# Optimization experiments

Hardware: AMD Instinct MI355X
Metric: run time of the kernel (lower is better)

The kernel has to match this reference:

```python
import jax, jax.numpy as jnp
import numpy as np

CHANNEL = 64
RATIO = 8
C1 = CHANNEL // RATIO


def setup_inputs() -> dict:
    key = jax.random.key(0)
    ks = jax.random.split(key, 8)
    b, c, h, w = 2, CHANNEL, 96, 96
    X = jax.random.normal(ks[0], (b, c, h, w), dtype=jnp.float32)
    Y = jax.random.normal(ks[1], (b, c, h, w), dtype=jnp.float32)
    # 1x1 conv weights (stored as [out, in]) + biases, Kaiming-ish scale
    s = 1.0 / np.sqrt(c)
    Wq = jax.random.uniform(ks[2], (C1, c), jnp.float32, -s, s)
    bq = jax.random.uniform(ks[3], (C1,), jnp.float32, -s, s)
    Wk = jax.random.uniform(ks[4], (C1, c), jnp.float32, -s, s)
    bk = jax.random.uniform(ks[5], (C1,), jnp.float32, -s, s)
    Wv = jax.random.uniform(ks[6], (c, c), jnp.float32, -s, s)
    bv = jax.random.uniform(ks[7], (c,), jnp.float32, -s, s)
    return {"X": X, "Y": Y, "Wq": Wq, "bq": bq, "Wk": Wk, "bk": bk, "Wv": Wv, "bv": bv}


def reference(X, Y, Wq, bq, Wk, bk, Wv, bv):
    b, c, h, w = Y.shape
    n = h * w
    # 1x1 convs as channel contractions -> [b, n, c_out]
    Xf = X.reshape(b, c, n)                       # [b, c, n]
    q = jnp.einsum('oc,bcn->bno', Wq, Xf) + bq    # [b, n, c1]
    k = jnp.einsum('oc,bcn->bno', Wk, Xf) + bk    # [b, n, c1]
    v = jnp.einsum('oc,bcn->bno', Wv, Y.reshape(b, c, n)) + bv  # [b, n, c]
    scores = jnp.einsum('bic,bjc->bij', q, k)     # [b, n, n]
    # NOTE: softmax over dim=1 (the first n axis), as in the original module
    a = jax.nn.softmax(scores, axis=1)
    x = jnp.einsum('bij,bjc->bic', a, v)          # [b, n, c]
    x = x.transpose(0, 2, 1).reshape(b, c, h, w)
    return Y + x
```

## Files before the change

### kernel.cpp

```cpp
#include <hip/hip_runtime.h>

#define NPOS 9216
#define NB 2
#define CCH 64
#define VZP 40

typedef __attribute__((ext_vector_type(8))) short short8;
typedef __attribute__((ext_vector_type(4))) float f32x4;

#define LOG2E 1.4426950408889634f

__device__ __forceinline__ ushort f2bf(float x) {
    unsigned u = __builtin_bit_cast(unsigned, x);
    u += 0x7FFFu + ((u >> 16) & 1u);
    return (ushort)(u >> 16);
}

__device__ __forceinline__ unsigned cvt_pk_bf16(float lo, float hi) {
    unsigned r;
    asm("v_cvt_pk_bf16_f32 %0, %1, %2" : "=v"(r) : "v"(lo), "v"(hi));
    return r;
}

__global__ __launch_bounds__(256) void qkv_kernel(
    const float* __restrict__ X, const float* __restrict__ Y,
    const float* __restrict__ Wq, const float* __restrict__ bq,
    const float* __restrict__ Wk, const float* __restrict__ bk,
    const float* __restrict__ Wv, const float* __restrict__ bv,
    ushort* __restrict__ qb, ushort* __restrict__ kb, float* __restrict__ v,
    float* __restrict__ out)
{
    __shared__ float wqkT[1024];
    __shared__ float wvT[4096];
    int tid = threadIdx.x;
    for (int idx = tid; idx < 1024; idx += 256) {
        int c = idx >> 4, o = idx & 15;
        wqkT[idx] = (o < 8) ? Wq[o * 64 + c] : Wk[(o - 8) * 64 + c];
    }
    for (int idx = tid; idx < 4096; idx += 256) {
        int c = idx >> 6, o = idx & 63;
        wvT[idx] = Wv[o * 64 + c];
    }
    __syncthreads();

    int p = tid & 63, s = tid >> 6;
    int base = blockIdx.x * 64;
    int b = base / NPOS;
    int n = (base % NPOS) + p;

    float va[16], qk[8];
    #pragma unroll
    for (int o = 0; o < 16; ++o) va[o] = bv[s * 16 + o];
    #pragma unroll
    for (int o = 0; o < 8; ++o) qk[o] = 0.f;
    if (s == 0) {
        #pragma unroll
        for (int o = 0; o < 8; ++o) qk[o] = bq[o];
    } else if (s == 1) {
        #pragma unroll
        for (int o = 0; o < 8; ++o) qk[o] = bk[o];
    }

    const float* Xb = X + (size_t)b * CCH * NPOS + n;
    const float* Yb = Y + (size_t)b * CCH * NPOS + n;
    float* ob = out + (size_t)b * CCH * NPOS + n;
    for (int c = 0; c < 64; ++c) {
        float yv = Yb[(size_t)c * NPOS];
        ob[(size_t)c * NPOS] = yv;
        const float4* wv4 = (const float4*)(wvT + c * 64 + s * 16);
        #pragma unroll
        for (int o4 = 0; o4 < 4; ++o4) {
            float4 wv = wv4[o4];
            va[o4*4+0] += wv.x * yv; va[o4*4+1] += wv.y * yv;
            va[o4*4+2] += wv.z * yv; va[o4*4+3] += wv.w * yv;
        }
        if (s < 2) {
            float xv = Xb[(size_t)c * NPOS];
            const float4* wq4 = (const float4*)(wqkT + c * 16 + s * 8);
            float4 w0 = wq4[0], w1 = wq4[1];
            qk[0] += w0.x * xv; qk[1] += w0.y * xv;
            qk[2] += w0.z * xv; qk[3] += w0.w * xv;
            qk[4] += w1.x * xv; qk[5] += w1.y * xv;
            qk[6] += w1.z * xv; qk[7] += w1.w * xv;
        }
    }
    float4* vdst = (float4*)(v + ((size_t)b * NPOS + n) * 64 + s * 16);
    #pragma unroll
    for (int o4 = 0; o4 < 4; ++o4)
        vdst[o4] = make_float4(va[o4*4], va[o4*4+1], va[o4*4+2], va[o4*4+3]);
    if (s < 2) {
        if (s == 0) {
            #pragma unroll
            for (int o = 0; o < 8; ++o) qk[o] *= LOG2E;
        }
        short8 row;
        #pragma unroll
        for (int o = 0; o < 8; ++o) row[o] = (short)f2bf(qk[o]);
        ushort* dst = (s == 0 ? qb : kb) + ((size_t)b * NPOS + n) * 8;
        *(short8*)dst = row;
    }
}

__global__ __launch_bounds__(256) void zpass_kernel(
    const ushort* __restrict__ qb, const ushort* __restrict__ kb,
    float* __restrict__ Z)
{
    int tid = threadIdx.x;
    int w = tid >> 6, l = tid & 63;
    int il = l & 15, g = l >> 4;
    int b = blockIdx.z;
    int jb = blockIdx.x * 64 + w * 16;
    const short8 zero8 = {0,0,0,0,0,0,0,0};
    const f32x4 cz = {0.f,0.f,0.f,0.f};

    short8 kf = zero8;
    if (g == 0) kf = *(const short8*)(kb + ((size_t)b * NPOS + jb + il) * 8);

    float za[4] = {0.f, 0.f, 0.f, 0.f};
    const ushort* qrow = qb + ((size_t)b * NPOS + blockIdx.y * 2304 + il) * 8;
    for (int is = 0; is < 144; ++is) {
        short8 qf = *(const short8*)(qrow + (size_t)is * 128);
        if (g != 0) qf = zero8;
        f32x4 sv = __builtin_amdgcn_mfma_f32_16x16x32_bf16(kf, qf, cz, 0, 0, 0);
        za[0] += __builtin_amdgcn_exp2f(sv[0]);
        za[1] += __builtin_amdgcn_exp2f(sv[1]);
        za[2] += __builtin_amdgcn_exp2f(sv[2]);
        za[3] += __builtin_amdgcn_exp2f(sv[3]);
    }
    #pragma unroll
    for (int r = 0; r < 4; ++r) {
        float x = za[r];
        x += __shfl_xor(x, 1, 16);
        x += __shfl_xor(x, 2, 16);
        x += __shfl_xor(x, 4, 16);
        x += __shfl_xor(x, 8, 16);
        za[r] = x;
    }
    if (il == 0) {
        #pragma unroll
        for (int r = 0; r < 4; ++r)
            atomicAdd(&Z[(size_t)b * NPOS + jb + g * 4 + r], za[r]);
    }
}

__global__ __launch_bounds__(256) void scalevT_kernel(
    const float* __restrict__ v, const float* __restrict__ Z,
    ushort* __restrict__ VzT)
{
    int tid = threadIdx.x;
    int p = tid & 63, s = tid >> 6;
    int base = blockIdx.x * 64;
    int b = base / NPOS;
    int n = (base % NPOS) + p;
    float rz = 1.0f / Z[(size_t)b * NPOS + n];
    const float4* vr = (const float4*)(v + ((size_t)b * NPOS + n) * 64 + s * 16);
    ushort* dst = VzT + (size_t)b * CCH * NPOS + n;
    #pragma unroll
    for (int q4 = 0; q4 < 4; ++q4) {
        float4 a = vr[q4];
        size_t c0 = s * 16 + q4 * 4;
        dst[(c0 + 0) * NPOS] = f2bf(a.x * rz);
        dst[(c0 + 1) * NPOS] = f2bf(a.y * rz);
        dst[(c0 + 2) * NPOS] = f2bf(a.z * rz);
        dst[(c0 + 3) * NPOS] = f2bf(a.w * rz);
    }
}

__global__ __launch_bounds__(256) void pass2_kernel(
    const ushort* __restrict__ qb, const ushort* __restrict__ kb,
    const ushort* __restrict__ VzT, float* __restrict__ out)
{
    __shared__ ushort vz_lds[2][64 * VZP];
    __shared__ ushort p_lds[4][512];
    int tid = threadIdx.x;
    int w = tid >> 6, l = tid & 63;
    int il = l & 15, g = l >> 4;
    int b = blockIdx.z;
    int ibase = blockIdx.x * 64 + w * 16;
    int j0 = blockIdx.y * 2304;

    const short8 zero8 = {0,0,0,0,0,0,0,0};
    const f32x4 cz = {0.f,0.f,0.f,0.f};

    short8 qf = zero8;
    if (g == 0) qf = *(const short8*)(qb + ((size_t)b * NPOS + ibase + il) * 8);

    f32x4 acc[4];
    #pragma unroll
    for (int cg = 0; cg < 4; ++cg) acc[cg] = cz;

    const ushort* kbb = kb + (size_t)b * NPOS * 8;
    int sc = tid >> 2, sslot = tid & 3;
    const ushort* vsrc = VzT + (size_t)b * CCH * NPOS + (size_t)sc * NPOS + j0 + sslot * 8;

    *(float4*)&vz_lds[0][sc * VZP + sslot * 8] = *(const float4*)vsrc;
    __syncthreads();

    int swz = (il >> 1) & 3;
    ushort* pw = p_lds[w];

    for (int st = 0; st < 72; ++st) {
        int jb = j0 + st * 32;
        int cur = st & 1;
        bool more = (st + 1) < 72;
        float4 nv = {0.f,0.f,0.f,0.f};
        if (more) nv = *(const float4*)(vsrc + (size_t)(st + 1) * 32);

        short8 kf0 = zero8, kf1 = zero8;
        if (g == 0) {
            kf0 = *(const short8*)(kbb + (size_t)(jb + il) * 8);
            kf1 = *(const short8*)(kbb + (size_t)(jb + 16 + il) * 8);
        }
        f32x4 s0 = __builtin_amdgcn_mfma_f32_16x16x32_bf16(kf0, qf, cz, 0, 0, 0);
        f32x4 s1 = __builtin_amdgcn_mfma_f32_16x16x32_bf16(kf1, qf, cz, 0, 0, 0);

        int rowoff = il * 32 + (g & 1) * 4;
        {
            int stored = ((g >> 1) ^ swz);
            unsigned u01 = cvt_pk_bf16(__builtin_amdgcn_exp2f(s0[0]),
                                       __builtin_amdgcn_exp2f(s0[1]));
            unsigned u23 = cvt_pk_bf16(__builtin_amdgcn_exp2f(s0[2]),
                                       __builtin_amdgcn_exp2f(s0[3]));
            *(unsigned*)&pw[rowoff + stored * 8 + 0] = u01;
            *(unsigned*)&pw[rowoff + stored * 8 + 2] = u23;
        }
        {
            int stored = ((2 | (g >> 1)) ^ swz);
            unsigned u01 = cvt_pk_bf16(__builtin_amdgcn_exp2f(s1[0]),
                                       __builtin_amdgcn_exp2f(s1[1]));
            unsigned u23 = cvt_pk_bf16(__builtin_amdgcn_exp2f(s1[2]),
                                       __builtin_amdgcn_exp2f(s1[3]));
            *(unsigned*)&pw[rowoff + stored * 8 + 0] = u01;
            *(unsigned*)&pw[rowoff + stored * 8 + 2] = u23;
        }

        short8 pf = *(short8*)&pw[il * 32 + ((g ^ swz) * 8)];

        #pragma unroll
        for (int cg = 0; cg < 4; ++cg) {
            short8 af = *(short8*)&vz_lds[cur][(cg * 16 + il) * VZP + g * 8];
            acc[cg] = __builtin_amdgcn_mfma_f32_16x16x32_bf16(af, pf, acc[cg], 0, 0, 0);
        }

        if (more) *(float4*)&vz_lds[cur ^ 1][sc * VZP + sslot * 8] = nv;
        __syncthreads();
    }

    float* ob = out + (size_t)b * CCH * NPOS + ibase + il;
    #pragma unroll
    for (int cg = 0; cg < 4; ++cg) {
        #pragma unroll
        for (int r = 0; r < 4; ++r) {
            int c = cg * 16 + g * 4 + r;
            atomicAdd(ob + (size_t)c * NPOS, acc[cg][r]);
        }
    }
}

extern "C" void kernel_launch(void* const* d_in, const int* in_sizes, int n_in,
                              void* d_out, int out_size, void* d_ws, size_t ws_size,
                              hipStream_t stream) {
    const float* X  = (const float*)d_in[0];
    const float* Y  = (const float*)d_in[1];
    const float* Wq = (const float*)d_in[2];
    const float* bq = (const float*)d_in[3];
    const float* Wk = (const float*)d_in[4];
    const float* bk = (const float*)d_in[5];
    const float* Wv = (const float*)d_in[6];
    const float* bv = (const float*)d_in[7];

    char* ws = (char*)d_ws;
    ushort* qb  = (ushort*)(ws);
    ushort* kbw = (ushort*)(ws + 294912);
    ushort* VzT = (ushort*)(ws + 589824);
    float*  v   = (float*) (ws + 2949120);
    float*  Z   = (float*) (ws + 7667712);

    hipMemsetAsync(Z, 0, (size_t)NB * NPOS * sizeof(float), stream);

    qkv_kernel<<<288, 256, 0, stream>>>(X, Y, Wq, bq, Wk, bk, Wv, bv,
                                        qb, kbw, v, (float*)d_out);
    zpass_kernel<<<dim3(144, 4, NB), 256, 0, stream>>>(qb, kbw, Z);
    scalevT_kernel<<<288, 256, 0, stream>>>(v, Z, VzT);
    pass2_kernel<<<dim3(144, 4, NB), 256, 0, stream>>>(qb, kbw, VzT, (float*)d_out);
}
```

Baseline: 207.6 us.

## Fold 1/Z into probabilities, widen pass2 tiles to 32 rows by 64 columns

V is now written directly as transposed bf16 by the QKV kernel, and the scale-by-1/Z step moves into pass2, where each exp score is multiplied by a precomputed reciprocal. This replaces the full scalevT pass and the fp32 V round trip with a tiny reciprocal kernel. pass2 now gives each wave 32 query rows over 64 j steps, using XOR-swizzled LDS tiles, prefetched K fragments and a split of 8 along j instead of 4. The larger tiles cut loop and sync overhead per MFMA, at the cost of more registers, more atomic adds per output and bf16 rounding applied to p/Z instead of V/Z.

New measurement: 218.9 us. 1.05x slower.

```diff
diff --git a/kernel.cpp b/kernel.cpp
--- a/kernel.cpp
+++ b/kernel.cpp
@@ -3,7 +3,9 @@
 #define NPOS 9216
 #define NB 2
 #define CCH 64
-#define VZP 40
+#define JSPLIT 8
+#define JCHUNK (NPOS / JSPLIT)
+#define NSTEP (JCHUNK / 64)
 
 typedef __attribute__((ext_vector_type(8))) short short8;
 typedef __attribute__((ext_vector_type(4))) float f32x4;
@@ -27,11 +29,11 @@
     const float* __restrict__ Wq, const float* __restrict__ bq,
     const float* __restrict__ Wk, const float* __restrict__ bk,
     const float* __restrict__ Wv, const float* __restrict__ bv,
-    ushort* __restrict__ qb, ushort* __restrict__ kb, float* __restrict__ v,
-    float* __restrict__ out)
+    ushort* __restrict__ qb, ushort* __restrict__ kb,
+    ushort* __restrict__ vT, float* __restrict__ out)
 {
     __shared__ float wqkT[1024];
-    __shared__ float wvT[4096];
+    __shared__ float wvTs[4096];
     int tid = threadIdx.x;
     for (int idx = tid; idx < 1024; idx += 256) {
         int c = idx >> 4, o = idx & 15;
@@ -39,7 +41,7 @@
     }
     for (int idx = tid; idx < 4096; idx += 256) {
         int c = idx >> 6, o = idx & 63;
-        wvT[idx] = Wv[o * 64 + c];
+        wvTs[idx] = Wv[o * 64 + c];
     }
     __syncthreads();
 
@@ -67,7 +69,7 @@
     for (int c = 0; c < 64; ++c) {
         float yv = Yb[(size_t)c * NPOS];
         ob[(size_t)c * NPOS] = yv;
-        const float4* wv4 = (const float4*)(wvT + c * 64 + s * 16);
+        const float4* wv4 = (const float4*)(wvTs + c * 64 + s * 16);
         #pragma unroll
         for (int o4 = 0; o4 < 4; ++o4) {
             float4 wv = wv4[o4];
@@ -84,10 +86,10 @@
             qk[6] += w1.z * xv; qk[7] += w1.w * xv;
         }
     }
-    float4* vdst = (float4*)(v + ((size_t)b * NPOS + n) * 64 + s * 16);
-    #pragma unroll
-    for (int o4 = 0; o4 < 4; ++o4)
-        vdst[o4] = make_float4(va[o4*4], va[o4*4+1], va[o4*4+2], va[o4*4+3]);
+    ushort* vdst = vT + (size_t)b * CCH * NPOS + n;
+    #pragma unroll
+    for (int o = 0; o < 16; ++o)
+        vdst[(size_t)(s * 16 + o) * NPOS] = f2bf(va[o]);
     if (s < 2) {
         if (s == 0) {
             #pragma unroll
@@ -118,6 +120,7 @@
 
     float za[4] = {0.f, 0.f, 0.f, 0.f};
     const ushort* qrow = qb + ((size_t)b * NPOS + blockIdx.y * 2304 + il) * 8;
+    #pragma unroll 4
     for (int is = 0; is < 144; ++is) {
         short8 qf = *(const short8*)(qrow + (size_t)is * 128);
         if (g != 0) qf = zero8;
@@ -143,118 +146,144 @@
     }
 }
 
-__global__ __launch_bounds__(256) void scalevT_kernel(
-    const float* __restrict__ v, const float* __restrict__ Z,
-    ushort* __restrict__ VzT)
+__global__ __launch_bounds__(256) void recipz_kernel(
+    const float* __restrict__ Z, float* __restrict__ rz)
 {
-    int tid = threadIdx.x;
-    int p = tid & 63, s = tid >> 6;
-    int base = blockIdx.x * 64;
-    int b = base / NPOS;
-    int n = (base % NPOS) + p;
-    float rz = 1.0f / Z[(size_t)b * NPOS + n];
-    const float4* vr = (const float4*)(v + ((size_t)b * NPOS + n) * 64 + s * 16);
-    ushort* dst = VzT + (size_t)b * CCH * NPOS + n;
-    #pragma unroll
-    for (int q4 = 0; q4 < 4; ++q4) {
-        float4 a = vr[q4];
-        size_t c0 = s * 16 + q4 * 4;
-        dst[(c0 + 0) * NPOS] = f2bf(a.x * rz);
-        dst[(c0 + 1) * NPOS] = f2bf(a.y * rz);
-        dst[(c0 + 2) * NPOS] = f2bf(a.z * rz);
-        dst[(c0 + 3) * NPOS] = f2bf(a.w * rz);
-    }
+    int i = blockIdx.x * 256 + threadIdx.x;
+    rz[i] = __builtin_amdgcn_rcpf(Z[i]);
 }
 
 __global__ __launch_bounds__(256) void pass2_kernel(
     const ushort* __restrict__ qb, const ushort* __restrict__ kb,
-    const ushort* __restrict__ VzT, float* __restrict__ out)
+    const ushort* __restrict__ vT, const float* __restrict__ rz,
+    float* __restrict__ out)
 {
-    __shared__ ushort vz_lds[2][64 * VZP];
-    __shared__ ushort p_lds[4][512];
+    __shared__ ushort vz_lds[2][64 * 64];
+    __shared__ ushort p_lds[4][32 * 64];
     int tid = threadIdx.x;
     int w = tid >> 6, l = tid & 63;
     int il = l & 15, g = l >> 4;
     int b = blockIdx.z;
-    int ibase = blockIdx.x * 64 + w * 16;
-    int j0 = blockIdx.y * 2304;
+    int ibase = blockIdx.x * 128 + w * 32;
+    int j0 = blockIdx.y * JCHUNK;
 
     const short8 zero8 = {0,0,0,0,0,0,0,0};
     const f32x4 cz = {0.f,0.f,0.f,0.f};
 
-    short8 qf = zero8;
-    if (g == 0) qf = *(const short8*)(qb + ((size_t)b * NPOS + ibase + il) * 8);
-
-    f32x4 acc[4];
-    #pragma unroll
-    for (int cg = 0; cg < 4; ++cg) acc[cg] = cz;
+    short8 qf0 = zero8, qf1 = zero8;
+    if (g == 0) {
+        qf0 = *(const short8*)(qb + ((size_t)b * NPOS + ibase + il) * 8);
+        qf1 = *(const short8*)(qb + ((size_t)b * NPOS + ibase + 16 + il) * 8);
+    }
+
+    f32x4 acc[2][4];
+    #pragma unroll
+    for (int h = 0; h < 2; ++h)
+        #pragma unroll
+        for (int cg = 0; cg < 4; ++cg) acc[h][cg] = cz;
 
     const ushort* kbb = kb + (size_t)b * NPOS * 8;
-    int sc = tid >> 2, sslot = tid & 3;
-    const ushort* vsrc = VzT + (size_t)b * CCH * NPOS + (size_t)sc * NPOS + j0 + sslot * 8;
-
-    *(float4*)&vz_lds[0][sc * VZP + sslot * 8] = *(const float4*)vsrc;
+    const float* rzb = rz + (size_t)b * NPOS;
+
+    int sr = tid >> 2, sq = tid & 3;
+    const ushort* vrow = vT + (size_t)b * CCH * NPOS + (size_t)sr * NPOS + j0;
+    int soff0 = (sq ^ (sr & 7)) * 8;
+    int soff1 = ((sq + 4) ^ (sr & 7)) * 8;
+    int xr = il & 7;
+
+    {
+        float4 ga = *(const float4*)(vrow + sq * 8);
+        float4 gb = *(const float4*)(vrow + (sq + 4) * 8);
+        *(float4*)&vz_lds[0][sr * 64 + soff0] = ga;
+        *(float4*)&vz_lds[0][sr * 64 + soff1] = gb;
+    }
+    short8 kf[4];
+    #pragma unroll
+    for (int t = 0; t < 4; ++t)
+        kf[t] = (g == 0) ? *(const short8*)(kbb + (size_t)(j0 + 16 * t + il) * 8)
+                         : zero8;
     __syncthreads();
 
-    int swz = (il >> 1) & 3;
     ushort* pw = p_lds[w];
 
-    for (int st = 0; st < 72; ++st) {
-        int jb = j0 + st * 32;
+    for (int st = 0; st < NSTEP; ++st) {
+        int jb = j0 + st * 64;
         int cur = st & 1;
-        bool more = (st + 1) < 72;
-        float4 nv = {0.f,0.f,0.f,0.f};
-        if (more) nv = *(const float4*)(vsrc + (size_t)(st + 1) * 32);
-
-        short8 kf0 = zero8, kf1 = zero8;
-        if (g == 0) {
-            kf0 = *(const short8*)(kbb + (size_t)(jb + il) * 8);
-            kf1 = *(const short8*)(kbb + (size_t)(jb + 16 + il) * 8);
-        }
-        f32x4 s0 = __builtin_amdgcn_mfma_f32_16x16x32_bf16(kf0, qf, cz, 0, 0, 0);
-        f32x4 s1 = __builtin_amdgcn_mfma_f32_16x16x32_bf16(kf1, qf, cz, 0, 0, 0);
-
-        int rowoff = il * 32 + (g & 1) * 4;
-        {
-            int stored = ((g >> 1) ^ swz);
-            unsigned u01 = cvt_pk_bf16(__builtin_amdgcn_exp2f(s0[0]),
-                                       __builtin_amdgcn_exp2f(s0[1]));
-            unsigned u23 = cvt_pk_bf16(__builtin_amdgcn_exp2f(s0[2]),
-                                       __builtin_amdgcn_exp2f(s0[3]));
-            *(unsigned*)&pw[rowoff + stored * 8 + 0] = u01;
-            *(unsigned*)&pw[rowoff + stored * 8 + 2] = u23;
-        }
-        {
-            int stored = ((2 | (g >> 1)) ^ swz);
-            unsigned u01 = cvt_pk_bf16(__builtin_amdgcn_exp2f(s1[0]),
-                                       __builtin_amdgcn_exp2f(s1[1]));
-            unsigned u23 = cvt_pk_bf16(__builtin_amdgcn_exp2f(s1[2]),
-                                       __builtin_amdgcn_exp2f(s1[3]));
-            *(unsigned*)&pw[rowoff + stored * 8 + 0] = u01;
-            *(unsigned*)&pw[rowoff + stored * 8 + 2] = u23;
-        }
-
-        short8 pf = *(short8*)&pw[il * 32 + ((g ^ swz) * 8)];
+        bool more = (st + 1) < NSTEP;
+
+        float4 g0n = {0,0,0,0}, g1n = {0,0,0,0};
+        short8 kn[4] = {zero8, zero8, zero8, zero8};
+        if (more) {
+            int jn = (st + 1) * 64;
+            g0n = *(const float4*)(vrow + jn + sq * 8);
+            g1n = *(const float4*)(vrow + jn + (sq + 4) * 8);
+            #pragma unroll
+            for (int t = 0; t < 4; ++t)
+                if (g == 0)
+                    kn[t] = *(const short8*)(kbb + (size_t)(jb + 64 + 16 * t + il) * 8);
+        }
+        float4 rzv[4];
+        #pragma unroll
+        for (int t = 0; t < 4; ++t)
+            rzv[t] = *(const float4*)(rzb + jb + 16 * t + 4 * g);
+
+        #pragma unroll
+        for (int h = 0; h < 2; ++h) {
+            short8 qf = h ? qf1 : qf0;
+            int rowoff = (16 * h + il) * 64;
+            #pragma unroll
+            for (int t = 0; t < 4; ++t) {
+                f32x4 sv = __builtin_amdgcn_mfma_f32_16x16x32_bf16(kf[t], qf, cz, 0, 0, 0);
+                float p0 = __builtin_amdgcn_exp2f(sv[0]) * rzv[t].x;
+                float p1 = __builtin_amdgcn_exp2f(sv[1]) * rzv[t].y;
+                float p2 = __builtin_amdgcn_exp2f(sv[2]) * rzv[t].z;
+                float p3 = __builtin_amdgcn_exp2f(sv[3]) * rzv[t].w;
+                uint2 u;
+                u.x = cvt_pk_bf16(p0, p1);
+                u.y = cvt_pk_bf16(p2, p3);
+                int stored = (2 * t + (g >> 1)) ^ xr;
+                *(uint2*)&pw[rowoff + stored * 8 + (g & 1) * 4] = u;
+            }
+        }
+
+        short8 pf[2][2];
+        #pragma unroll
+        for (int h = 0; h < 2; ++h) {
+            int rowoff = (16 * h + il) * 64;
+            pf[h][0] = *(short8*)&pw[rowoff + ((g ^ xr) * 8)];
+            pf[h][1] = *(short8*)&pw[rowoff + (((4 + g) ^ xr) * 8)];
+        }
 
         #pragma unroll
         for (int cg = 0; cg < 4; ++cg) {
-            short8 af = *(short8*)&vz_lds[cur][(cg * 16 + il) * VZP + g * 8];
-            acc[cg] = __builtin_amdgcn_mfma_f32_16x16x32_bf16(af, pf, acc[cg], 0, 0, 0);
-        }
-
-        if (more) *(float4*)&vz_lds[cur ^ 1][sc * VZP + sslot * 8] = nv;
+            int row = (cg * 16 + il) * 64;
+            short8 af0 = *(short8*)&vz_lds[cur][row + ((g ^ xr) * 8)];
+            short8 af1 = *(short8*)&vz_lds[cur][row + (((4 + g) ^ xr) * 8)];
+            #pragma unroll
+            for (int h = 0; h < 2; ++h) {
+                acc[h][cg] = __builtin_amdgcn_mfma_f32_16x16x32_bf16(af0, pf[h][0], acc[h][cg], 0, 0, 0);
+                acc[h][cg] = __builtin_amdgcn_mfma_f32_16x16x32_bf16(af1, pf[h][1], acc[h][cg], 0, 0, 0);
+            }
+        }
+
+        if (more) {
+            *(float4*)&vz_lds[cur ^ 1][sr * 64 + soff0] = g0n;
+            *(float4*)&vz_lds[cur ^ 1][sr * 64 + soff1] = g1n;
+            #pragma unroll
+            for (int t = 0; t < 4; ++t) kf[t] = kn[t];
+        }
         __syncthreads();
     }
 
     float* ob = out + (size_t)b * CCH * NPOS + ibase + il;
     #pragma unroll
-    for (int cg = 0; cg < 4; ++cg) {
-        #pragma unroll
-        for (int r = 0; r < 4; ++r) {
-            int c = cg * 16 + g * 4 + r;
-            atomicAdd(ob + (size_t)c * NPOS, acc[cg][r]);
-        }
-    }
+    for (int h = 0; h < 2; ++h)
+        #pragma unroll
+        for (int cg = 0; cg < 4; ++cg)
+            #pragma unroll
+            for (int r = 0; r < 4; ++r)
+                atomicAdd(ob + (size_t)(cg * 16 + g * 4 + r) * NPOS + 16 * h,
+                          acc[h][cg][r]);
 }
 
 extern "C" void kernel_launch(void* const* d_in, const int* in_sizes, int n_in,
@@ -272,15 +301,16 @@
     char* ws = (char*)d_ws;
     ushort* qb  = (ushort*)(ws);
     ushort* kbw = (ushort*)(ws + 294912);
-    ushort* VzT = (ushort*)(ws + 589824);
-    float*  v   = (float*) (ws + 2949120);
-    float*  Z   = (float*) (ws + 7667712);
+    ushort* vT  = (ushort*)(ws + 589824);
+    float*  Z   = (float*) (ws + 2949120);
+    float*  rz  = (float*) (ws + 3022848);
 
     hipMemsetAsync(Z, 0, (size_t)NB * NPOS * sizeof(float), stream);
 
     qkv_kernel<<<288, 256, 0, stream>>>(X, Y, Wq, bq, Wk, bk, Wv, bv,
-                                        qb, kbw, v, (float*)d_out);
+                                        qb, kbw, vT, (float*)d_out);
     zpass_kernel<<<dim3(144, 4, NB), 256, 0, stream>>>(qb, kbw, Z);
-    scalevT_kernel<<<288, 256, 0, stream>>>(v, Z, VzT);
-    pass2_kernel<<<dim3(144, 4, NB), 256, 0, stream>>>(qb, kbw, VzT, (float*)d_out);
-}
+    recipz_kernel<<<72, 256, 0, stream>>>(Z, rz);
+    pass2_kernel<<<dim3(72, JSPLIT, NB), 256, 0, stream>>>(qb, kbw, vT, rz,
+                                                           (float*)d_out);
+}
```
